# Kernel optimization log

Measured on AMD Instinct MI355X. Metric: run time of the kernel, lower is better.

## Reference

```python
import jax, jax.numpy as jnp
import numpy as np

N = 100000
IN_CH = 128
OUT_CH = 40
K = 2
E = 3200000


def setup_inputs() -> dict:
    key = jax.random.key(0)
    k1, k2, k3, k4 = jax.random.split(key, 4)
    x = jax.random.normal(k1, (N, IN_CH), dtype=jnp.float32)
    edge_index = jax.random.randint(k2, (2, E), 0, N, dtype=jnp.int64)
    # Linear params (PyG Linear: glorot-style init approximated)
    scale = 1.0 / np.sqrt(IN_CH)
    W = jax.random.uniform(k3, (IN_CH, OUT_CH), dtype=jnp.float32, minval=-scale, maxval=scale)
    b = jax.random.uniform(k4, (OUT_CH,), dtype=jnp.float32, minval=-scale, maxval=scale)
    return {"x": x, "edge_index": edge_index, "W": W, "b": b}


def reference(x, edge_index, W, b):
    n = x.shape[0]
    row, col = edge_index[0], edge_index[1]  # source -> target
    # gcn_norm: add self loops, symmetric normalization
    loop = jnp.arange(n, dtype=row.dtype)
    row = jnp.concatenate([row, loop])
    col = jnp.concatenate([col, loop])
    ones = jnp.ones(row.shape[0], dtype=x.dtype)
    deg = jax.ops.segment_sum(ones, col, num_segments=n)  # in-degree incl. self-loop
    deg_inv_sqrt = jnp.where(deg > 0, jax.lax.rsqrt(deg), 0.0)
    norm = deg_inv_sqrt[row] * deg_inv_sqrt[col]  # [E+N]
    h = x
    for _ in range(K):
        # sparse SpMM: out[col] += norm * h[row]
        h = jax.ops.segment_sum(norm[:, None] * h[row], col, num_segments=n)
    logits = h @ W + b
    return jax.nn.log_softmax(logits, axis=-1)
```

## Files before the change

### kernel.cpp

```cpp
#include <hip/hip_runtime.h>
#include <hip/hip_fp16.h>
#include <math.h>

#define NN 100000
#define ICH 128
#define OCH 40
#define NE 3200000
#define BSH 8
#define BNODES 256
#define BMASK 255
#define NB 391
#define CAP 9216
#define TILE 4096
#define NBIN ((NE + TILE - 1) / TILE)
#define YSTRIDE 40
#define YU2 (YSTRIDE / 8)
#define XWBLK 1563

typedef __attribute__((ext_vector_type(2))) float floatx2;
typedef __attribute__((ext_vector_type(4))) float floatx4;
typedef __attribute__((ext_vector_type(8))) short bf16x8;

__device__ __forceinline__ unsigned int pk_bf16(float a, float b) {
    unsigned int r;
    asm("v_cvt_pk_bf16_f32 %0, %1, %2" : "=v"(r) : "v"(a), "v"(b));
    return r;
}

__device__ __forceinline__ void acc_fp8x8(const uint2 u, float* acc) {
    floatx2 p0 = __builtin_amdgcn_cvt_pk_f32_fp8((int)u.x, false);
    floatx2 p1 = __builtin_amdgcn_cvt_pk_f32_fp8((int)u.x, true);
    floatx2 p2 = __builtin_amdgcn_cvt_pk_f32_fp8((int)u.y, false);
    floatx2 p3 = __builtin_amdgcn_cvt_pk_f32_fp8((int)u.y, true);
    acc[0] += p0.x; acc[1] += p0.y; acc[2] += p1.x; acc[3] += p1.y;
    acc[4] += p2.x; acc[5] += p2.y; acc[6] += p3.x; acc[7] += p3.y;
}

__device__ __forceinline__ uint2 pack_fp8x8(const float* v) {
    int lo = 0, hi = 0;
    lo = __builtin_amdgcn_cvt_pk_fp8_f32(v[0], v[1], lo, false);
    lo = __builtin_amdgcn_cvt_pk_fp8_f32(v[2], v[3], lo, true);
    hi = __builtin_amdgcn_cvt_pk_fp8_f32(v[4], v[5], hi, false);
    hi = __builtin_amdgcn_cvt_pk_fp8_f32(v[6], v[7], hi, true);
    return make_uint2((unsigned int)lo, (unsigned int)hi);
}

__device__ __forceinline__ void row_gather(const int* __restrict__ csr, int kb, int ke, int q,
                                           const uint2* __restrict__ base, float* acc) {
    int k = kb;
    if (k + 8 <= ke) {
        int s[8];
        uint2 v[8];
#pragma unroll
        for (int j = 0; j < 8; ++j) s[j] = csr[k + j];
#pragma unroll
        for (int j = 0; j < 8; ++j) v[j] = base[(size_t)s[j] * YU2 + q];
        k += 8;
        for (; k + 8 <= ke; k += 8) {
            int s2[8];
            uint2 w[8];
#pragma unroll
            for (int j = 0; j < 8; ++j) s2[j] = csr[k + j];
#pragma unroll
            for (int j = 0; j < 8; ++j) w[j] = base[(size_t)s2[j] * YU2 + q];
#pragma unroll
            for (int j = 0; j < 8; ++j) acc_fp8x8(v[j], acc);
#pragma unroll
            for (int j = 0; j < 8; ++j) v[j] = w[j];
        }
#pragma unroll
        for (int j = 0; j < 8; ++j) acc_fp8x8(v[j], acc);
    }
    for (; k < ke; ++k) acc_fp8x8(base[(size_t)csr[k] * YU2 + q], acc);
}

__global__ __launch_bounds__(512) void k_bin(const int* __restrict__ ei, int* __restrict__ bcursor,
                                             unsigned int* __restrict__ packed) {
    __shared__ unsigned int entries[TILE];
    __shared__ unsigned short bid[TILE];
    __shared__ int hist[512], base[512], gbase[512], cur[512];
    int t = threadIdx.x;
    int tile0 = blockIdx.x * TILE;
    int tcnt = min(TILE, NE - tile0);
    hist[t] = 0;
    __syncthreads();
    int src[8], dst[8];
#pragma unroll
    for (int i = 0; i < 8; ++i) {
        int l = t + i * 512;
        if (l < tcnt) {
            int e = tile0 + l;
            src[i] = ei[e];
            dst[i] = ei[NE + e];
            atomicAdd(&hist[dst[i] >> BSH], 1);
        } else dst[i] = -1;
    }
    __syncthreads();
    int own = hist[t];
    base[t] = own;
    __syncthreads();
    for (int off = 1; off < 512; off <<= 1) {
        int v = (t >= off) ? base[t - off] : 0;
        __syncthreads();
        base[t] += v;
        __syncthreads();
    }
    int excl = base[t] - own;
    __syncthreads();
    base[t] = excl;
    cur[t] = excl;
    if (t < NB && own > 0) gbase[t] = atomicAdd(&bcursor[t], own);
    __syncthreads();
#pragma unroll
    for (int i = 0; i < 8; ++i) {
        if (dst[i] >= 0) {
            int bb = dst[i] >> BSH;
            int pos = atomicAdd(&cur[bb], 1);
            entries[pos] = ((unsigned int)(dst[i] & BMASK) << 17) | (unsigned int)src[i];
            bid[pos] = (unsigned short)bb;
        }
    }
    __syncthreads();
    for (int l = t; l < tcnt; l += 512) {
        int bb = bid[l];
        packed[(size_t)bb * CAP + gbase[bb] + (l - base[bb])] = entries[l];
    }
}

__global__ __launch_bounds__(512) void k_bscan(const int* __restrict__ bcursor, int* __restrict__ bbase,
                                               int* __restrict__ rowptr, const float* __restrict__ W,
                                               unsigned int* __restrict__ wbf) {
    __shared__ int s[512];
    int t = threadIdx.x;
    int v = (t < NB) ? bcursor[t] : 0;
    s[t] = v;
    __syncthreads();
    for (int off = 1; off < 512; off <<= 1) {
        int u = (t >= off) ? s[t - off] : 0;
        __syncthreads();
        s[t] += u;
        __syncthreads();
    }
    if (t < NB) bbase[t] = s[t] - v;
    if (t == 0) rowptr[NN] = NE;
    for (int e = t; e < 1536; e += 512) {
        int hs = e / 768;
        int rem = e - hs * 768;
        int ss = rem / 192;
        int rem2 = rem - ss * 192;
        int n = rem2 >> 6;
        int lane = rem2 & 63;
        int kbase = ss * 32 + (lane >> 4) * 8;
        int col = n * 16 + (lane & 15);
        unsigned int u4[4];
#pragma unroll
        for (int p = 0; p < 4; ++p) {
            float f0 = (col < OCH) ? W[(size_t)(kbase + 2 * p) * OCH + col] : 0.f;
            float f1 = (col < OCH) ? W[(size_t)(kbase + 2 * p + 1) * OCH + col] : 0.f;
            unsigned int h = pk_bf16(f0, f1);
            if (hs == 0) {
                u4[p] = h;
            } else {
                float l0 = f0 - __uint_as_float(h << 16);
                float l1 = f1 - __uint_as_float(h & 0xFFFF0000u);
                u4[p] = pk_bf16(l0, l1);
            }
        }
        ((uint4*)wbf)[e] = make_uint4(u4[0], u4[1], u4[2], u4[3]);
    }
}

__global__ __launch_bounds__(512) void k_csr(const int* __restrict__ bcursor, const int* __restrict__ bbase,
                                             const unsigned int* __restrict__ packed,
                                             int* __restrict__ rowptr, float* __restrict__ dis,
                                             int* __restrict__ csr) {
    __shared__ unsigned int ent[CAP];
    __shared__ int hist[BNODES], cur[BNODES], ps[BNODES];
    int b = blockIdx.x;
    int t = threadIdx.x;
    int cnt = bcursor[b];
    int cbase = bbase[b];
    int node0 = b << BSH;
    int nn = min(BNODES, NN - node0);
    if (t < BNODES) hist[t] = 0;
    __syncthreads();
    const unsigned int* pk = packed + (size_t)b * CAP;
    for (int l = t; l < cnt; l += 512) {
        unsigned int e = pk[l];
        ent[l] = e;
        atomicAdd(&hist[e >> 17], 1);
    }
    __syncthreads();
    if (t < BNODES) ps[t] = hist[t];
    __syncthreads();
    for (int off = 1; off < BNODES; off <<= 1) {
        int u = (t >= off && t < BNODES) ? ps[t - off] : 0;
        __syncthreads();
        if (t < BNODES) ps[t] += u;
        __syncthreads();
    }
    if (t < BNODES) {
        int excl = ps[t] - hist[t];
        cur[t] = excl;
        if (t < nn) {
            rowptr[node0 + t] = cbase + excl;
            dis[node0 + t] = rsqrtf((float)hist[t] + 1.0f);
        }
    }
    __syncthreads();
    for (int l = t; l < cnt; l += 512) {
        unsigned int e = ent[l];
        int pos = atomicAdd(&cur[e >> 17], 1);
        csr[cbase + pos] = (int)(e & 0x1FFFF);
    }
}

__global__ __launch_bounds__(128) void k_xw(const float* __restrict__ x, const unsigned int* __restrict__ wbf,
                                            const float* __restrict__ dis, unsigned char* __restrict__ y0) {
    int t = threadIdx.x;
    int wid = t >> 6, lane = t & 63;
    const bf16x8* wf = (const bf16x8*)wbf;
    bf16x8 whi[4][3], wlo[4][3];
#pragma unroll
    for (int s = 0; s < 4; ++s)
#pragma unroll
        for (int n = 0; n < 3; ++n) {
            whi[s][n] = wf[(s * 3 + n) * 64 + lane];
            wlo[s][n] = wf[768 / 1 * 0 + (768) + 0 * 64 - 768 + (1 * 768) + (s * 3 + n) * 64 + lane];
        }
    int rbase = blockIdx.x * 64 + wid * 32;
#pragma unroll
    for (int tt = 0; tt < 2; ++tt) {
        int r0 = rbase + tt * 16;
        int rowa = r0 + (lane & 15);
        int rowc = min(rowa, NN - 1);
        int kb = (lane >> 4) * 8;
        const float4* xp = (const float4*)(x + (size_t)rowc * ICH + kb);
        float4 xa[4][2];
#pragma unroll
        for (int s = 0; s < 4; ++s) {
            xa[s][0] = xp[s * 8];
            xa[s][1] = xp[s * 8 + 1];
        }
        floatx4 acc[3] = {{0.f, 0.f, 0.f, 0.f}, {0.f, 0.f, 0.f, 0.f}, {0.f, 0.f, 0.f, 0.f}};
#pragma unroll
        for (int s = 0; s < 4; ++s) {
            float f[8] = {xa[s][0].x, xa[s][0].y, xa[s][0].z, xa[s][0].w,
                          xa[s][1].x, xa[s][1].y, xa[s][1].z, xa[s][1].w};
            union { unsigned int u[4]; bf16x8 v; } ah, al;
#pragma unroll
            for (int p = 0; p < 4; ++p) {
                unsigned int h = pk_bf16(f[2 * p], f[2 * p + 1]);
                ah.u[p] = h;
                float l0 = f[2 * p] - __uint_as_float(h << 16);
                float l1 = f[2 * p + 1] - __uint_as_float(h & 0xFFFF0000u);
                al.u[p] = pk_bf16(l0, l1);
            }
#pragma unroll
            for (int n = 0; n < 3; ++n) {
                acc[n] = __builtin_amdgcn_mfma_f32_16x16x32_bf16(ah.v, whi[s][n], acc[n], 0, 0, 0);
                acc[n] = __builtin_amdgcn_mfma_f32_16x16x32_bf16(al.v, whi[s][n], acc[n], 0, 0, 0);
                acc[n] = __builtin_amdgcn_mfma_f32_16x16x32_bf16(ah.v, wlo[s][n], acc[n], 0, 0, 0);
            }
        }
        int rc0 = r0 + (lane >> 4) * 4;
        float dd[4];
#pragma unroll
        for (int r = 0; r < 4; ++r) dd[r] = (rc0 + r < NN) ? dis[rc0 + r] : 0.f;
#pragma unroll
        for (int n = 0; n < 3; ++n) {
            int col = n * 16 + (lane & 15);
            if (col < OCH) {
#pragma unroll
                for (int r = 0; r < 4; ++r) {
                    int row = rc0 + r;
                    if (row < NN) {
                        float val = acc[n][r] * dd[r];
                        int p8 = __builtin_amdgcn_cvt_pk_fp8_f32(val, val, 0, false);
                        y0[(size_t)row * YSTRIDE + col] = (unsigned char)(p8 & 0xFF);
                    }
                }
            }
        }
    }
}

__global__ __launch_bounds__(256) void k_hop1(const int* __restrict__ rowptr, const int* __restrict__ csr,
                                              const float* __restrict__ dis, const unsigned char* __restrict__ y0,
                                              unsigned char* __restrict__ y1) {
    int g = blockIdx.x * 256 + threadIdx.x;
    if (g >= NN * 5) return;
    int i = g / 5, q = g - 5 * i;
    const uint2* base = (const uint2*)y0;
    float acc[8];
#pragma unroll
    for (int j = 0; j < 8; ++j) acc[j] = 0.f;
    acc_fp8x8(base[(size_t)i * YU2 + q], acc);
    row_gather(csr, rowptr[i], rowptr[i + 1], q, base, acc);
    float d = dis[i], d2 = d * d;
#pragma unroll
    for (int j = 0; j < 8; ++j) acc[j] *= d2;
    ((uint2*)y1)[(size_t)i * YU2 + q] = pack_fp8x8(acc);
}

__global__ __launch_bounds__(320) void k_hop2f(const int* __restrict__ rowptr, const int* __restrict__ csr,
                                               const float* __restrict__ dis, const unsigned char* __restrict__ y1,
                                               const float* __restrict__ b, float* __restrict__ out) {
    __shared__ float red[64][5];
    int tid = threadIdx.x;
    int lg = tid / 5;
    int q = tid - 5 * lg;
    int g = blockIdx.x * 64 + lg;
    bool active = (g < NN);
    float l[8];
    if (active) {
        const uint2* base = (const uint2*)y1;
        float acc[8];
#pragma unroll
        for (int j = 0; j < 8; ++j) acc[j] = 0.f;
        acc_fp8x8(base[(size_t)g * YU2 + q], acc);
        row_gather(csr, rowptr[g], rowptr[g + 1], q, base, acc);
        float d = dis[g];
#pragma unroll
        for (int j = 0; j < 8; ++j) l[j] = d * acc[j] + b[8 * q + j];
    } else {
#pragma unroll
        for (int j = 0; j < 8; ++j) l[j] = -1e30f;
    }
    float m8 = l[0];
#pragma unroll
    for (int j = 1; j < 8; ++j) m8 = fmaxf(m8, l[j]);
    red[lg][q] = m8;
    __syncthreads();
    float gm = red[lg][0];
#pragma unroll
    for (int j = 1; j < 5; ++j) gm = fmaxf(gm, red[lg][j]);
    __syncthreads();
    float s8 = 0.f;
#pragma unroll
    for (int j = 0; j < 8; ++j) s8 += __expf(l[j] - gm);
    red[lg][q] = s8;
    __syncthreads();
    float gs = red[lg][0];
#pragma unroll
    for (int j = 1; j < 5; ++j) gs += red[lg][j];
    float ls = __logf(gs) + gm;
    if (active) {
        floatx4* orow = (floatx4*)(out + (size_t)g * OCH + 8 * q);
        floatx4 o0 = {l[0] - ls, l[1] - ls, l[2] - ls, l[3] - ls};
        floatx4 o1 = {l[4] - ls, l[5] - ls, l[6] - ls, l[7] - ls};
        __builtin_nontemporal_store(o0, orow);
        __builtin_nontemporal_store(o1, orow + 1);
    }
}

extern "C" void kernel_launch(void* const* d_in, const int* in_sizes, int n_in,
                              void* d_out, int out_size, void* d_ws, size_t ws_size,
                              hipStream_t stream) {
    const float* x  = (const float*)d_in[0];
    const int*   ei = (const int*)d_in[1];
    const float* W  = (const float*)d_in[2];
    const float* b  = (const float*)d_in[3];
    float* out = (float*)d_out;

    char* ws = (char*)d_ws;
    int*           bcursor = (int*)(ws + 0);
    int*           bbase   = (int*)(ws + 2048);
    int*           rowptr  = (int*)(ws + 4096);
    float*         dis     = (float*)(ws + 409600);
    unsigned int*  wbf     = (unsigned int*)(ws + 811008);
    unsigned int*  packed  = (unsigned int*)(ws + 843776);
    unsigned char* y0      = (unsigned char*)(ws + 843776);
    unsigned char* y1      = (unsigned char*)(ws + 4849664);
    int*           csr     = (int*)(ws + 15261696);

    hipMemsetAsync(bcursor, 0, NB * sizeof(int), stream);
    k_bin<<<NBIN, 512, 0, stream>>>(ei, bcursor, packed);
    k_bscan<<<1, 512, 0, stream>>>(bcursor, bbase, rowptr, W, wbf);
    k_csr<<<NB, 512, 0, stream>>>(bcursor, bbase, packed, rowptr, dis, csr);
    k_xw<<<XWBLK, 128, 0, stream>>>(x, wbf, dis, y0);
    k_hop1<<<(NN * 5 + 255) / 256, 256, 0, stream>>>(rowptr, csr, dis, y0, y1);
    k_hop2f<<<(NN + 63) / 64, 320, 0, stream>>>(rowptr, csr, dis, y1, b, out);
}
```

Baseline: 245.5 us.

## Pad fp8 feature rows to 48 bytes and gather with 16-byte loads

After: 281.4 us. 1.15x slower.

```diff
diff --git a/kernel.cpp b/kernel.cpp
--- a/kernel.cpp
+++ b/kernel.cpp
@@ -13,8 +13,7 @@
 #define CAP 9216
 #define TILE 4096
 #define NBIN ((NE + TILE - 1) / TILE)
-#define YSTRIDE 40
-#define YU2 (YSTRIDE / 8)
+#define YSTRIDE 48
 #define XWBLK 1563
 
 typedef __attribute__((ext_vector_type(2))) float floatx2;
@@ -27,13 +26,18 @@
     return r;
 }
 
-__device__ __forceinline__ void acc_fp8x8(const uint2 u, float* acc) {
-    floatx2 p0 = __builtin_amdgcn_cvt_pk_f32_fp8((int)u.x, false);
-    floatx2 p1 = __builtin_amdgcn_cvt_pk_f32_fp8((int)u.x, true);
-    floatx2 p2 = __builtin_amdgcn_cvt_pk_f32_fp8((int)u.y, false);
-    floatx2 p3 = __builtin_amdgcn_cvt_pk_f32_fp8((int)u.y, true);
+__device__ __forceinline__ void acc_fp8x8(unsigned int ux, unsigned int uy, float* acc) {
+    floatx2 p0 = __builtin_amdgcn_cvt_pk_f32_fp8((int)ux, false);
+    floatx2 p1 = __builtin_amdgcn_cvt_pk_f32_fp8((int)ux, true);
+    floatx2 p2 = __builtin_amdgcn_cvt_pk_f32_fp8((int)uy, false);
+    floatx2 p3 = __builtin_amdgcn_cvt_pk_f32_fp8((int)uy, true);
     acc[0] += p0.x; acc[1] += p0.y; acc[2] += p1.x; acc[3] += p1.y;
     acc[4] += p2.x; acc[5] += p2.y; acc[6] += p3.x; acc[7] += p3.y;
+}
+
+__device__ __forceinline__ void acc_fp8x16(const uint4 u, float* acc) {
+    acc_fp8x8(u.x, u.y, acc);
+    acc_fp8x8(u.z, u.w, acc + 8);
 }
 
 __device__ __forceinline__ uint2 pack_fp8x8(const float* v) {
@@ -45,33 +49,33 @@
     return make_uint2((unsigned int)lo, (unsigned int)hi);
 }
 
-__device__ __forceinline__ void row_gather(const int* __restrict__ csr, int kb, int ke, int q,
-                                           const uint2* __restrict__ base, float* acc) {
+__device__ __forceinline__ void row_gather16(const int* __restrict__ csr, int kb, int ke,
+                                             const uint4* __restrict__ p4, float* acc) {
     int k = kb;
     if (k + 8 <= ke) {
         int s[8];
-        uint2 v[8];
+        uint4 v[8];
 #pragma unroll
         for (int j = 0; j < 8; ++j) s[j] = csr[k + j];
 #pragma unroll
-        for (int j = 0; j < 8; ++j) v[j] = base[(size_t)s[j] * YU2 + q];
+        for (int j = 0; j < 8; ++j) v[j] = p4[(size_t)s[j] * 3];
         k += 8;
         for (; k + 8 <= ke; k += 8) {
             int s2[8];
-            uint2 w[8];
+            uint4 w[8];
 #pragma unroll
             for (int j = 0; j < 8; ++j) s2[j] = csr[k + j];
 #pragma unroll
-            for (int j = 0; j < 8; ++j) w[j] = base[(size_t)s2[j] * YU2 + q];
-#pragma unroll
-            for (int j = 0; j < 8; ++j) acc_fp8x8(v[j], acc);
+            for (int j = 0; j < 8; ++j) w[j] = p4[(size_t)s2[j] * 3];
+#pragma unroll
+            for (int j = 0; j < 8; ++j) acc_fp8x16(v[j], acc);
 #pragma unroll
             for (int j = 0; j < 8; ++j) v[j] = w[j];
         }
 #pragma unroll
-        for (int j = 0; j < 8; ++j) acc_fp8x8(v[j], acc);
-    }
-    for (; k < ke; ++k) acc_fp8x8(base[(size_t)csr[k] * YU2 + q], acc);
+        for (int j = 0; j < 8; ++j) acc_fp8x16(v[j], acc);
+    }
+    for (; k < ke; ++k) acc_fp8x16(p4[(size_t)csr[k] * 3], acc);
 }
 
 __global__ __launch_bounds__(512) void k_bin(const int* __restrict__ ei, int* __restrict__ bcursor,
@@ -226,7 +230,7 @@
 #pragma unroll
         for (int n = 0; n < 3; ++n) {
             whi[s][n] = wf[(s * 3 + n) * 64 + lane];
-            wlo[s][n] = wf[768 / 1 * 0 + (768) + 0 * 64 - 768 + (1 * 768) + (s * 3 + n) * 64 + lane];
+            wlo[s][n] = wf[768 + (s * 3 + n) * 64 + lane];
         }
     int rbase = blockIdx.x * 64 + wid * 32;
 #pragma unroll
@@ -289,68 +293,72 @@
                                               const float* __restrict__ dis, const unsigned char* __restrict__ y0,
                                               unsigned char* __restrict__ y1) {
     int g = blockIdx.x * 256 + threadIdx.x;
-    if (g >= NN * 5) return;
-    int i = g / 5, q = g - 5 * i;
-    const uint2* base = (const uint2*)y0;
-    float acc[8];
-#pragma unroll
-    for (int j = 0; j < 8; ++j) acc[j] = 0.f;
-    acc_fp8x8(base[(size_t)i * YU2 + q], acc);
-    row_gather(csr, rowptr[i], rowptr[i + 1], q, base, acc);
+    if (g >= NN * 3) return;
+    int i = g / 3, q = g - 3 * i;
+    const uint4* p4 = (const uint4*)(y0 + q * 16);
+    float acc[16];
+#pragma unroll
+    for (int j = 0; j < 16; ++j) acc[j] = 0.f;
+    acc_fp8x16(p4[(size_t)i * 3], acc);
+    row_gather16(csr, rowptr[i], rowptr[i + 1], p4, acc);
     float d = dis[i], d2 = d * d;
 #pragma unroll
-    for (int j = 0; j < 8; ++j) acc[j] *= d2;
-    ((uint2*)y1)[(size_t)i * YU2 + q] = pack_fp8x8(acc);
-}
-
-__global__ __launch_bounds__(320) void k_hop2f(const int* __restrict__ rowptr, const int* __restrict__ csr,
+    for (int j = 0; j < 16; ++j) acc[j] *= d2;
+    if (q < 2) {
+        uint2 a = pack_fp8x8(acc), b = pack_fp8x8(acc + 8);
+        ((uint4*)(y1 + (size_t)i * YSTRIDE))[q] = make_uint4(a.x, a.y, b.x, b.y);
+    } else {
+        uint2 a = pack_fp8x8(acc);
+        *(uint2*)(y1 + (size_t)i * YSTRIDE + 32) = a;
+    }
+}
+
+__global__ __launch_bounds__(384) void k_hop2f(const int* __restrict__ rowptr, const int* __restrict__ csr,
                                                const float* __restrict__ dis, const unsigned char* __restrict__ y1,
                                                const float* __restrict__ b, float* __restrict__ out) {
-    __shared__ float red[64][5];
+    __shared__ float red[128][3];
     int tid = threadIdx.x;
-    int lg = tid / 5;
-    int q = tid - 5 * lg;
-    int g = blockIdx.x * 64 + lg;
+    int lg = tid / 3;
+    int q = tid - 3 * lg;
+    int g = blockIdx.x * 128 + lg;
     bool active = (g < NN);
-    float l[8];
+    float l[16];
     if (active) {
-        const uint2* base = (const uint2*)y1;
-        float acc[8];
-#pragma unroll
-        for (int j = 0; j < 8; ++j) acc[j] = 0.f;
-        acc_fp8x8(base[(size_t)g * YU2 + q], acc);
-        row_gather(csr, rowptr[g], rowptr[g + 1], q, base, acc);
+        const uint4* p4 = (const uint4*)(y1 + q * 16);
+        float acc[16];
+#pragma unroll
+        for (int j = 0; j < 16; ++j) acc[j] = 0.f;
+        acc_fp8x16(p4[(size_t)g * 3], acc);
+        row_gather16(csr, rowptr[g], rowptr[g + 1], p4, acc);
         float d = dis[g];
-#pragma unroll
-        for (int j = 0; j < 8; ++j) l[j] = d * acc[j] + b[8 * q + j];
+        int nch = (q == 2) ? 8 : 16;
+#pragma unroll
+        for (int j = 0; j < 16; ++j) l[j] = (j < nch) ? (d * acc[j] + b[16 * q + j]) : -1e30f;
     } else {
 #pragma unroll
-        for (int j = 0; j < 8; ++j) l[j] = -1e30f;
-    }
-    float m8 = l[0];
-#pragma unroll
-    for (int j = 1; j < 8; ++j) m8 = fmaxf(m8, l[j]);
-    red[lg][q] = m8;
-    __syncthreads();
-    float gm = red[lg][0];
-#pragma unroll
-    for (int j = 1; j < 5; ++j) gm = fmaxf(gm, red[lg][j]);
-    __syncthreads();
-    float s8 = 0.f;
-#pragma unroll
-    for (int j = 0; j < 8; ++j) s8 += __expf(l[j] - gm);
-    red[lg][q] = s8;
-    __syncthreads();
-    float gs = red[lg][0];
-#pragma unroll
-    for (int j = 1; j < 5; ++j) gs += red[lg][j];
+        for (int j = 0; j < 16; ++j) l[j] = -1e30f;
+    }
+    float m16 = l[0];
+#pragma unroll
+    for (int j = 1; j < 16; ++j) m16 = fmaxf(m16, l[j]);
+    red[lg][q] = m16;
+    __syncthreads();
+    float gm = fmaxf(fmaxf(red[lg][0], red[lg][1]), red[lg][2]);
+    __syncthreads();
+    float s16 = 0.f;
+#pragma unroll
+    for (int j = 0; j < 16; ++j) s16 += __expf(l[j] - gm);
+    red[lg][q] = s16;
+    __syncthreads();
+    float gs = red[lg][0] + red[lg][1] + red[lg][2];
     float ls = __logf(gs) + gm;
     if (active) {
-        floatx4* orow = (floatx4*)(out + (size_t)g * OCH + 8 * q);
-        floatx4 o0 = {l[0] - ls, l[1] - ls, l[2] - ls, l[3] - ls};
-        floatx4 o1 = {l[4] - ls, l[5] - ls, l[6] - ls, l[7] - ls};
-        __builtin_nontemporal_store(o0, orow);
-        __builtin_nontemporal_store(o1, orow + 1);
+        int nst = (q == 2) ? 2 : 4;
+        floatx4* orow = (floatx4*)(out + (size_t)g * OCH + q * 16);
+        for (int j4 = 0; j4 < nst; ++j4) {
+            floatx4 o = {l[4 * j4] - ls, l[4 * j4 + 1] - ls, l[4 * j4 + 2] - ls, l[4 * j4 + 3] - ls};
+            __builtin_nontemporal_store(o, orow + j4);
+        }
     }
 }
 
@@ -371,7 +379,7 @@
     unsigned int*  wbf     = (unsigned int*)(ws + 811008);
     unsigned int*  packed  = (unsigned int*)(ws + 843776);
     unsigned char* y0      = (unsigned char*)(ws + 843776);
-    unsigned char* y1      = (unsigned char*)(ws + 4849664);
+    unsigned char* y1      = (unsigned char*)(ws + 5643776);
     int*           csr     = (int*)(ws + 15261696);
 
     hipMemsetAsync(bcursor, 0, NB * sizeof(int), stream);
@@ -379,6 +387,6 @@
     k_bscan<<<1, 512, 0, stream>>>(bcursor, bbase, rowptr, W, wbf);
     k_csr<<<NB, 512, 0, stream>>>(bcursor, bbase, packed, rowptr, dis, csr);
     k_xw<<<XWBLK, 128, 0, stream>>>(x, wbf, dis, y0);
-    k_hop1<<<(NN * 5 + 255) / 256, 256, 0, stream>>>(rowptr, csr, dis, y0, y1);
-    k_hop2f<<<(NN + 63) / 64, 320, 0, stream>>>(rowptr, csr, dis, y1, b, out);
-}
+    k_hop1<<<(NN * 3 + 255) / 256, 256, 0, stream>>>(rowptr, csr, dis, y0, y1);
+    k_hop2f<<<(NN + 127) / 128, 384, 0, stream>>>(rowptr, csr, dis, y1, b, out);
+}
```
